# Optimization experiments

Hardware: AMD Instinct MI355X
Metric: run time of the kernel (lower is better)

The kernel has to match this reference:

```python
import jax, jax.numpy as jnp
import numpy as np

V, D, L, H, SLOTS, FF = 32000, 1024, 6, 16, 4096, 4096
DH = D // H

def rmsnorm(x, w, eps=1e-8):
    return x * jax.lax.rsqrt(jnp.mean(x * x, axis=-1, keepdims=True) + eps) * w

def rope(x):
    # x: [B,T,D]; interleaved RoPE over full d_model as in RoPEEmbedding
    T = x.shape[1]
    inv_freq = 1.0 / (10000.0 ** (jnp.arange(0, D, 2, dtype=jnp.float32) / D))
    freqs = jnp.arange(T, dtype=jnp.float32)[:, None] * inv_freq[None, :]  # [T, D/2]
    cos, sin = jnp.cos(freqs), jnp.sin(freqs)
    x1, x2 = x[..., ::2], x[..., 1::2]
    out = jnp.stack([x1 * cos - x2 * sin, x1 * sin + x2 * cos], axis=-1)
    return out.reshape(x.shape)

def block(x, Wq, Wk, Wv, Wo, bo, n1, Wg, Wu, Wd, n2):
    B, T, _ = x.shape
    q = (x @ Wq).reshape(B, T, H, DH)
    k = (x @ Wk).reshape(B, T, H, DH)
    v = (x @ Wv).reshape(B, T, H, DH)
    scores = jnp.einsum('bqhd,bkhd->bhqk', q, k) * (DH ** -0.5)
    attn = jax.nn.softmax(scores, axis=-1)
    o = jnp.einsum('bhqk,bkhd->bqhd', attn, v).reshape(B, T, D)
    x = rmsnorm(x + o @ Wo + bo, n1)
    ff = (jax.nn.silu(x @ Wg) * (x @ Wu)) @ Wd
    return rmsnorm(x + ff, n2)

def setup_inputs() -> dict:
    key = jax.random.key(0)
    ks = jax.random.split(key, 20)
    nrm = lambda k, s: (jax.random.normal(k, s, jnp.float32) * 0.02)
    inp = {
        'ids': jax.random.randint(ks[0], (2, 2048), 0, V),
        'tok_embed': nrm(ks[1], (V, D)),
        'Wq': nrm(ks[2], (L, D, D)), 'Wk': nrm(ks[3], (L, D, D)),
        'Wv': nrm(ks[4], (L, D, D)), 'Wo': nrm(ks[5], (L, D, D)),
        'bo': jnp.zeros((L, D), jnp.float32),
        'n1': jnp.ones((L, D), jnp.float32),
        'Wg': nrm(ks[6], (L, D, FF)), 'Wu': nrm(ks[7], (L, D, FF)),
        'Wd': nrm(ks[8], (L, FF, D)),
        'n2': jnp.ones((L, D), jnp.float32),
        'mem': nrm(ks[9], (SLOTS, D)),
        'Wsp': nrm(ks[10], (D, D)), 'bsp': jnp.zeros((D,), jnp.float32),
        'Wrp': nrm(ks[11], (D, D)), 'brp': jnp.zeros((D,), jnp.float32),
        'nout': jnp.ones((D,), jnp.float32),
    }
    return inp

def reference(ids, tok_embed, Wq, Wk, Wv, Wo, bo, n1, Wg, Wu, Wd, n2,
              mem, Wsp, bsp, Wrp, brp, nout):
    x = tok_embed[ids]            # [B,T,D] gather
    x = rope(x)
    for i in range(L):
        x = block(x, Wq[i], Wk[i], Wv[i], Wo[i], bo[i], n1[i],
                  Wg[i], Wu[i], Wd[i], n2[i])
    # StateBank content-addressed read: route queries over memory slots
    q = x @ Wsp + bsp                                   # [B,T,D]
    slot_scores = jnp.einsum('btd,sd->bts', q, mem) * (D ** -0.5)
    attention_maps = jax.nn.softmax(slot_scores, axis=-1)  # [B,T,SLOTS]
    r = jnp.einsum('bts,sd->btd', attention_maps, mem)     # gather-route read
    r = r @ Wrp + brp
    h = rmsnorm(x + r, nout)
    logits = h @ tok_embed.T      # tied lm_head
    return logits
```

## Files before the change

kernel.cpp:

```cpp
#include <hip/hip_runtime.h>

typedef __bf16 bf16;
typedef __attribute__((ext_vector_type(8))) __bf16 bf16x8;
typedef __attribute__((ext_vector_type(4))) __bf16 bf16x4;
typedef __attribute__((ext_vector_type(4))) float f32x4;

#define NL 6
#define DIM 1024
#define NH 16
#define DH 64
#define TT 2048
#define BB 2
#define BT 4096
#define FFD 4096
#define NSLOT 4096
#define NV 32000

__device__ __forceinline__ void gld16(const void* g, void* l) {
  __builtin_amdgcn_global_load_lds(
      (const __attribute__((address_space(1))) void*)g,
      (__attribute__((address_space(3))) void*)l, 16, 0, 0);
}


__global__ void cvt_bf16(const float* __restrict__ s, bf16* __restrict__ d, long n) {
  long i = ((long)blockIdx.x * 256 + threadIdx.x) * 4;
  if (i + 3 < n) {
    float4 v = *(const float4*)(s + i);
    bf16x4 o = {(bf16)v.x, (bf16)v.y, (bf16)v.z, (bf16)v.w};
    *(bf16x4*)(d + i) = o;
  }
}

__global__ void transpose_cvt(const float* __restrict__ src, bf16* __restrict__ dst, int R, int C) {
  __shared__ float tile[32][33];
  int c0 = blockIdx.x * 32, r0 = blockIdx.y * 32;
  int tx = threadIdx.x, ty = threadIdx.y;
#pragma unroll
  for (int i = 0; i < 4; ++i)
    tile[ty + i * 8][tx] = src[(size_t)(r0 + ty + i * 8) * C + c0 + tx];
  __syncthreads();
#pragma unroll
  for (int i = 0; i < 4; ++i)
    dst[(size_t)(c0 + ty + i * 8) * R + r0 + tx] = (bf16)tile[tx][ty + i * 8];
}

__global__ void transpose_v(const bf16* __restrict__ v, int ldv, bf16* __restrict__ vT) {
  __shared__ bf16 tile[32][33];
  int t0 = blockIdx.x * 32, d0 = blockIdx.y * 32, bh = blockIdx.z;
  int b = bh >> 4, h = bh & 15;
  int tx = threadIdx.x, ty = threadIdx.y;
#pragma unroll
  for (int i = 0; i < 4; ++i)
    tile[ty + i * 8][tx] = v[(size_t)(b * TT + t0 + ty + i * 8) * ldv + h * DH + d0 + tx];
  __syncthreads();
#pragma unroll
  for (int i = 0; i < 4; ++i)
    vT[((size_t)bh * DH + d0 + ty + i * 8) * TT + t0 + tx] = tile[tx][ty + i * 8];
}


__global__ void embed_rope(const int* __restrict__ ids, const float* __restrict__ emb,
                           float* __restrict__ xf, bf16* __restrict__ xb) {
  int bt = blockIdx.x;
  int t = bt & (TT - 1);
  int id = ids[bt];
  const float* row = emb + (size_t)id * DIM;
  for (int p = threadIdx.x; p < DIM / 2; p += 256) {
    float x1 = row[2 * p], x2 = row[2 * p + 1];
    float inv = __expf(-9.210340371976184f * (float)p * (1.0f / 512.0f));
    float ang = (float)t * inv;
    float c = cosf(ang), s = sinf(ang);
    float o1 = x1 * c - x2 * s;
    float o2 = x1 * s + x2 * c;
    size_t base = (size_t)bt * DIM + 2 * p;
    xf[base] = o1; xf[base + 1] = o2;
    xb[base] = (bf16)o1; xb[base + 1] = (bf16)o2;
  }
}


enum { EP_BF16 = 0, EP_F32 = 1, EP_F32_BIAS = 2, EP_BF16_BIAS = 3, EP_SILU_MUL = 4 };

template <int BM, int BN, int WMW, int WNW, int EP>
__global__ __launch_bounds__(WMW * WNW * 64, 2) void gemmk(
    const bf16* __restrict__ A, const bf16* __restrict__ Bt, void* __restrict__ Cp,
    const float* __restrict__ bias, const bf16* __restrict__ aux,
    int M, int N, int K) {
  constexpr int BK = 32;
  constexpr int NWAVE = WMW * WNW;
  constexpr int NTHR = NWAVE * 64;
  constexpr int MF = BM / (WMW * 16);
  constexpr int NF = BN / (WNW * 16);
  constexpr int AE = BM * BK;
  constexpr int BE = BN * BK;
  constexpr int RHALF = NTHR / 4;
  __shared__ bf16 sA[4][AE];
  __shared__ bf16 sB[4][BE];

  const int tid = threadIdx.x;
  const int lane = tid & 63;
  const int r16 = lane & 15, hi = lane >> 4;
  const int wave = tid >> 6;
  const int wm = wave / WNW, wn = wave % WNW;

  const int nwg = gridDim.x;
  const int orig = blockIdx.x;
  const int qq = nwg >> 3, rr = nwg & 7;
  const int xcd = orig & 7, cidx = orig >> 3;
  const int wg = (xcd < rr ? xcd * (qq + 1) : rr * (qq + 1) + (xcd - rr) * qq) + cidx;
  const int gM = M / BM;
  const int m0 = (wg % gM) * BM;
  const int n0 = (wg / gM) * BN;

  const int srow = tid >> 2;
  const int ccol = tid & 3;
  const int skey = (srow >> 1) & 3;
  const int gcol = ((ccol ^ skey)) * 8;
  const bf16* aS = A + (size_t)(m0 + srow) * K + gcol;
  const bf16* bS = Bt + (size_t)(n0 + srow) * K + gcol;
  const int dst0 = srow * BK + ccol * 8;

  const int rkey = (r16 >> 1) & 3;
  const int rchunk = (hi ^ rkey) * 8;

  f32x4 acc[MF][NF] = {};
  const int NT = K / BK;

  gld16(aS, &sA[0][dst0]);
  gld16(aS + (size_t)RHALF * K, &sA[0][dst0 + RHALF * BK]);
  gld16(bS, &sB[0][dst0]);
  gld16(bS + (size_t)RHALF * K, &sB[0][dst0 + RHALF * BK]);
  gld16(aS + BK, &sA[1][dst0]);
  gld16(aS + BK + (size_t)RHALF * K, &sA[1][dst0 + RHALF * BK]);
  gld16(bS + BK, &sB[1][dst0]);
  gld16(bS + BK + (size_t)RHALF * K, &sB[1][dst0 + RHALF * BK]);

  for (int t = 0; t < NT; ++t) {
    const int cb = t & 3;
    const int pb = (t + 2) & 3;
    const bool pre = (t + 2) < NT;
    if (pre) {
      gld16(aS + (size_t)(t + 2) * BK, &sA[pb][dst0]);
      gld16(aS + (size_t)(t + 2) * BK + (size_t)RHALF * K, &sA[pb][dst0 + RHALF * BK]);
    }
    if (pre)             asm volatile("s_waitcnt vmcnt(6)" ::: "memory");
    else if (t + 1 < NT) asm volatile("s_waitcnt vmcnt(4)" ::: "memory");
    else                 asm volatile("s_waitcnt vmcnt(0)" ::: "memory");
    __builtin_amdgcn_s_barrier();
    __builtin_amdgcn_sched_barrier(0);

    bf16x8 bf_[NF];
#pragma unroll
    for (int j = 0; j < NF; ++j)
      bf_[j] = *(const bf16x8*)&sB[cb][(wn * (NF * 16) + j * 16 + r16) * BK + rchunk];
    if (pre) {
      gld16(bS + (size_t)(t + 2) * BK, &sB[pb][dst0]);
      gld16(bS + (size_t)(t + 2) * BK + (size_t)RHALF * K, &sB[pb][dst0 + RHALF * BK]);
    }
    bf16x8 af[MF];
#pragma unroll
    for (int i = 0; i < MF; ++i)
      af[i] = *(const bf16x8*)&sA[cb][(wm * (MF * 16) + i * 16 + r16) * BK + rchunk];
    __builtin_amdgcn_s_setprio(1);
#pragma unroll
    for (int i = 0; i < MF; ++i)
#pragma unroll
      for (int j = 0; j < NF; ++j)
        acc[i][j] = __builtin_amdgcn_mfma_f32_16x16x32_bf16(af[i], bf_[j], acc[i][j], 0, 0, 0);
    __builtin_amdgcn_s_setprio(0);
  }

#pragma unroll
  for (int i = 0; i < MF; ++i) {
    const int m = m0 + wm * (MF * 16) + i * 16 + hi * 4;
#pragma unroll
    for (int j = 0; j < NF; ++j) {
      const int n = n0 + wn * (NF * 16) + j * 16 + r16;
#pragma unroll
      for (int q = 0; q < 4; ++q) {
        size_t idx = (size_t)(m + q) * N + n;
        float v = acc[i][j][q];
        if constexpr (EP == EP_F32) {
          ((float*)Cp)[idx] = v;
        } else if constexpr (EP == EP_F32_BIAS) {
          ((float*)Cp)[idx] = v + bias[n];
        } else if constexpr (EP == EP_BF16) {
          ((bf16*)Cp)[idx] = (bf16)v;
        } else if constexpr (EP == EP_BF16_BIAS) {
          ((bf16*)Cp)[idx] = (bf16)(v + bias[n]);
        } else {
          float sg = v / (1.0f + __expf(-v));
          ((bf16*)Cp)[idx] = (bf16)(sg * (float)aux[idx]);
        }
      }
    }
  }
}


__global__ __launch_bounds__(256, 2) void attn_flash(
    const bf16* __restrict__ Qp, const bf16* __restrict__ Kp, int ldk,
    const bf16* __restrict__ Vt, bf16* __restrict__ Op) {
  __shared__ bf16 Ks[2][128 * 32];
  __shared__ bf16 Vs[4][64 * 32];
  __shared__ bf16 Ps[4][4][16 * 40];
  const int tid = threadIdx.x, lane = tid & 63, wave = tid >> 6;
  const int h = blockIdx.y, b = blockIdx.z;
  const int r16 = lane & 15, hi = lane >> 4;
  const int qrow = blockIdx.x * 64 + wave * 16 + r16;

  bf16x8 qa[2];
  {
    const bf16* qp = Qp + (size_t)(b * TT + qrow) * ldk + h * DH + hi * 8;
    qa[0] = *(const bf16x8*)qp;
    qa[1] = *(const bf16x8*)(qp + 32);
  }
  const bf16* kBase = Kp + (size_t)(b * TT) * ldk + h * DH;
  const bf16* vBase = Vt + (size_t)(b * NH + h) * DH * TT;

  const int srow = tid >> 2, ccol = tid & 3;
  const int skey = (srow >> 1) & 3;
  const int scolS = (ccol ^ skey) * 8;
  const int dstc = ccol * 8;
  const int rkey = (r16 >> 1) & 3;
  const int rchunk = (hi ^ rkey) * 8;

  float m_run[4] = {-1e30f, -1e30f, -1e30f, -1e30f};
  float l_run[4] = {0.f, 0.f, 0.f, 0.f};
  f32x4 oacc[4] = {};

  for (int kt = 0; kt < TT; kt += 128) {
#pragma unroll
    for (int half = 0; half < 2; ++half) {
      gld16(kBase + (size_t)(kt + srow) * ldk + half * 32 + scolS, &Ks[half][srow * 32 + dstc]);
      gld16(kBase + (size_t)(kt + 64 + srow) * ldk + half * 32 + scolS, &Ks[half][(64 + srow) * 32 + dstc]);
    }
#pragma unroll
    for (int ks = 0; ks < 4; ++ks)
      gld16(vBase + (size_t)srow * TT + kt + ks * 32 + scolS, &Vs[ks][srow * 32 + dstc]);
    __syncthreads();

    f32x4 s[8];
#pragma unroll
    for (int kg = 0; kg < 8; ++kg) {
      f32x4 z = {};
      bf16x8 kb0 = *(const bf16x8*)&Ks[0][(kg * 16 + r16) * 32 + rchunk];
      bf16x8 kb1 = *(const bf16x8*)&Ks[1][(kg * 16 + r16) * 32 + rchunk];
      z = __builtin_amdgcn_mfma_f32_16x16x32_bf16(qa[0], kb0, z, 0, 0, 0);
      z = __builtin_amdgcn_mfma_f32_16x16x32_bf16(qa[1], kb1, z, 0, 0, 0);
      s[kg] = z * 0.125f;
    }
#pragma unroll
    for (int i = 0; i < 4; ++i) {
      float pm = s[0][i];
#pragma unroll
      for (int kg = 1; kg < 8; ++kg) pm = fmaxf(pm, s[kg][i]);
      pm = fmaxf(pm, __shfl_xor(pm, 1));
      pm = fmaxf(pm, __shfl_xor(pm, 2));
      pm = fmaxf(pm, __shfl_xor(pm, 4));
      pm = fmaxf(pm, __shfl_xor(pm, 8));
      float mnew = fmaxf(m_run[i], pm);
      float sc = __expf(m_run[i] - mnew);
      m_run[i] = mnew;
      l_run[i] *= sc;
#pragma unroll
      for (int n = 0; n < 4; ++n) oacc[n][i] *= sc;
#pragma unroll
      for (int kg = 0; kg < 8; ++kg) {
        float p = __expf(s[kg][i] - mnew);
        l_run[i] += p;
        Ps[wave][kg >> 1][(hi * 4 + i) * 40 + (kg & 1) * 16 + r16] = (bf16)p;
      }
    }
#pragma unroll
    for (int ks = 0; ks < 4; ++ks) {
      bf16x8 pa = *(const bf16x8*)&Ps[wave][ks][r16 * 40 + hi * 8];
#pragma unroll
      for (int n = 0; n < 4; ++n) {
        bf16x8 vb = *(const bf16x8*)&Vs[ks][(n * 16 + r16) * 32 + rchunk];
        oacc[n] = __builtin_amdgcn_mfma_f32_16x16x32_bf16(pa, vb, oacc[n], 0, 0, 0);
      }
    }
    __syncthreads();
  }

#pragma unroll
  for (int i = 0; i < 4; ++i) {
    float l = l_run[i];
    l += __shfl_xor(l, 1);
    l += __shfl_xor(l, 2);
    l += __shfl_xor(l, 4);
    l += __shfl_xor(l, 8);
    float inv = 1.0f / l;
    int trow = blockIdx.x * 64 + wave * 16 + hi * 4 + i;
    size_t base = ((size_t)b * TT + trow) * DIM + h * DH;
#pragma unroll
    for (int n = 0; n < 4; ++n)
      Op[base + n * 16 + r16] = (bf16)(oacc[n][i] * inv);
  }
}


__global__ __launch_bounds__(256) void resid_rms(
    const float* __restrict__ xin, const float* __restrict__ y, const float* __restrict__ wgt,
    float* __restrict__ xf_out, bf16* __restrict__ xb_out) {
  __shared__ float red[4];
  const int r = blockIdx.x, tid = threadIdx.x;
  const size_t base = (size_t)r * DIM + tid * 4;
  float4 v = *(const float4*)(xin + base);
  float4 u = *(const float4*)(y + base);
  v.x += u.x; v.y += u.y; v.z += u.z; v.w += u.w;
  float ss = v.x * v.x + v.y * v.y + v.z * v.z + v.w * v.w;
#pragma unroll
  for (int d = 1; d < 64; d <<= 1) ss += __shfl_xor(ss, d);
  if ((tid & 63) == 0) red[tid >> 6] = ss;
  __syncthreads();
  ss = red[0] + red[1] + red[2] + red[3];
  float sc = rsqrtf(ss * (1.0f / DIM) + 1e-8f);
  const float4 wv = *(const float4*)(wgt + tid * 4);
  float o0 = v.x * sc * wv.x, o1 = v.y * sc * wv.y, o2 = v.z * sc * wv.z, o3 = v.w * sc * wv.w;
  if (xf_out) {
    float4 ov = {o0, o1, o2, o3};
    *(float4*)(xf_out + base) = ov;
  }
  bf16x4 ob = {(bf16)o0, (bf16)o1, (bf16)o2, (bf16)o3};
  *(bf16x4*)(xb_out + base) = ob;
}


__global__ __launch_bounds__(256) void softmax_rows(const float* __restrict__ Sc, bf16* __restrict__ P) {
  __shared__ float red[4];
  const int r = blockIdx.x, tid = threadIdx.x;
  const float* row = Sc + (size_t)r * NSLOT;
  float4 v[4];
#pragma unroll
  for (int i = 0; i < 4; ++i) v[i] = *(const float4*)(row + tid * 4 + i * 1024);
  float mx = -1e30f;
#pragma unroll
  for (int i = 0; i < 4; ++i)
    mx = fmaxf(fmaxf(fmaxf(fmaxf(mx, v[i].x), v[i].y), v[i].z), v[i].w);
#pragma unroll
  for (int d = 1; d < 64; d <<= 1) mx = fmaxf(mx, __shfl_xor(mx, d));
  if ((tid & 63) == 0) red[tid >> 6] = mx;
  __syncthreads();
  mx = fmaxf(fmaxf(red[0], red[1]), fmaxf(red[2], red[3]));
  __syncthreads();
  float e[16];
  float sum = 0.f;
#pragma unroll
  for (int i = 0; i < 4; ++i) {
    e[i * 4 + 0] = __expf((v[i].x - mx) * 0.03125f);
    e[i * 4 + 1] = __expf((v[i].y - mx) * 0.03125f);
    e[i * 4 + 2] = __expf((v[i].z - mx) * 0.03125f);
    e[i * 4 + 3] = __expf((v[i].w - mx) * 0.03125f);
    sum += e[i * 4 + 0] + e[i * 4 + 1] + e[i * 4 + 2] + e[i * 4 + 3];
  }
#pragma unroll
  for (int d = 1; d < 64; d <<= 1) sum += __shfl_xor(sum, d);
  if ((tid & 63) == 0) red[tid >> 6] = sum;
  __syncthreads();
  sum = red[0] + red[1] + red[2] + red[3];
  float inv = 1.0f / sum;
#pragma unroll
  for (int i = 0; i < 4; ++i) {
    bf16x4 ob = {(bf16)(e[i * 4 + 0] * inv), (bf16)(e[i * 4 + 1] * inv),
                 (bf16)(e[i * 4 + 2] * inv), (bf16)(e[i * 4 + 3] * inv)};
    *(bf16x4*)(P + (size_t)r * NSLOT + tid * 4 + i * 1024) = ob;
  }
}


extern "C" void kernel_launch(void* const* d_in, const int* in_sizes, int n_in,
                              void* d_out, int out_size, void* d_ws, size_t ws_size,
                              hipStream_t stream) {
  (void)in_sizes; (void)n_in; (void)out_size;
  const int* ids = (const int*)d_in[0];
  const float* emb = (const float*)d_in[1];
  const float* Wq = (const float*)d_in[2];
  const float* Wk = (const float*)d_in[3];
  const float* Wv = (const float*)d_in[4];
  const float* Wo = (const float*)d_in[5];
  const float* bo = (const float*)d_in[6];
  const float* n1 = (const float*)d_in[7];
  const float* Wg = (const float*)d_in[8];
  const float* Wu = (const float*)d_in[9];
  const float* Wd = (const float*)d_in[10];
  const float* n2 = (const float*)d_in[11];
  const float* memp = (const float*)d_in[12];
  const float* Wsp = (const float*)d_in[13];
  const float* bsp = (const float*)d_in[14];
  const float* Wrp = (const float*)d_in[15];
  const float* brp = (const float*)d_in[16];
  const float* nout = (const float*)d_in[17];

  char* w = (char*)d_ws;
  auto alloc = [&](size_t bytes) -> void* {
    void* p = (void*)w;
    w += (bytes + 255) & ~(size_t)255;
    return p;
  };

  const size_t dd = (size_t)DIM * DIM;
  const size_t dff = (size_t)DIM * FFD;

  bf16* tok_b = (bf16*)alloc((size_t)NV * DIM * 2);
  bf16* mem_b = (bf16*)alloc((size_t)NSLOT * DIM * 2);
  bf16* memT  = (bf16*)alloc((size_t)NSLOT * DIM * 2);
  bf16* WspT  = (bf16*)alloc(dd * 2);
  bf16* WrpT  = (bf16*)alloc(dd * 2);
  float* xf   = (float*)alloc((size_t)BT * DIM * 4);
  bf16* xb    = (bf16*)alloc((size_t)BT * DIM * 2);
  float* yb   = (float*)alloc((size_t)BT * DIM * 4);
  bf16* W3T   = (bf16*)alloc(3 * dd * 2);
  bf16* WoT   = (bf16*)alloc(dd * 2);
  bf16* WgT   = (bf16*)alloc(dff * 2);
  bf16* WuT   = (bf16*)alloc(dff * 2);
  bf16* WdT   = (bf16*)alloc(dff * 2);
  bf16* qkv   = (bf16*)alloc((size_t)BT * 3 * DIM * 2);
  bf16* vT_   = (bf16*)alloc((size_t)BT * DIM * 2);
  bf16* ot_   = (bf16*)alloc((size_t)BT * DIM * 2);
  bf16* qb    = (bf16*)alloc((size_t)BT * DIM * 2);
  bf16* rb    = (bf16*)alloc((size_t)BT * DIM * 2);
  bf16* hb    = (bf16*)alloc((size_t)BT * DIM * 2);

  size_t used = (size_t)(w - (char*)d_ws);
  size_t region_bytes = (size_t)BT * NSLOT * 4 + (size_t)BT * NSLOT * 2;
  char* region;
  if (used + region_bytes <= ws_size) region = (char*)alloc(region_bytes);
  else region = (char*)d_out;
  bf16* Ub = (bf16*)region;
  bf16* Hb = (bf16*)(region + (size_t)BT * FFD * 2);
  float* scoresF = (float*)region;
  bf16* attnb = (bf16*)(region + (size_t)BT * NSLOT * 4);

  dim3 blkT(32, 8);

  cvt_bf16<<<NV * DIM / 1024, 256, 0, stream>>>(emb, tok_b, (long)NV * DIM);
  cvt_bf16<<<NSLOT * DIM / 1024, 256, 0, stream>>>(memp, mem_b, (long)NSLOT * DIM);
  transpose_cvt<<<dim3(DIM / 32, NSLOT / 32), blkT, 0, stream>>>(memp, memT, NSLOT, DIM);
  transpose_cvt<<<dim3(DIM / 32, DIM / 32), blkT, 0, stream>>>(Wsp, WspT, DIM, DIM);
  transpose_cvt<<<dim3(DIM / 32, DIM / 32), blkT, 0, stream>>>(Wrp, WrpT, DIM, DIM);
  embed_rope<<<BT, 256, 0, stream>>>(ids, emb, xf, xb);

  for (int l = 0; l < NL; ++l) {
    transpose_cvt<<<dim3(32, 32), blkT, 0, stream>>>(Wq + l * dd, W3T, DIM, DIM);
    transpose_cvt<<<dim3(32, 32), blkT, 0, stream>>>(Wk + l * dd, W3T + dd, DIM, DIM);
    transpose_cvt<<<dim3(32, 32), blkT, 0, stream>>>(Wv + l * dd, W3T + 2 * dd, DIM, DIM);
    transpose_cvt<<<dim3(32, 32), blkT, 0, stream>>>(Wo + l * dd, WoT, DIM, DIM);
    transpose_cvt<<<dim3(FFD / 32, DIM / 32), blkT, 0, stream>>>(Wg + l * dff, WgT, DIM, FFD);
    transpose_cvt<<<dim3(FFD / 32, DIM / 32), blkT, 0, stream>>>(Wu + l * dff, WuT, DIM, FFD);
    transpose_cvt<<<dim3(DIM / 32, FFD / 32), blkT, 0, stream>>>(Wd + l * dff, WdT, FFD, DIM);

    gemmk<128, 128, 2, 2, EP_BF16><<<dim3(32 * 24), 256, 0, stream>>>(
        xb, W3T, qkv, nullptr, nullptr, BT, 3 * DIM, DIM);
    transpose_v<<<dim3(TT / 32, DH / 32, BB * NH), blkT, 0, stream>>>(qkv + 2 * DIM, 3 * DIM, vT_);
    attn_flash<<<dim3(TT / 64, NH, BB), 256, 0, stream>>>(qkv, qkv + DIM, 3 * DIM, vT_, ot_);
    gemmk<128, 128, 2, 2, EP_F32_BIAS><<<dim3(8 * 32), 256, 0, stream>>>(
        ot_, WoT, yb, bo + l * DIM, nullptr, BT, DIM, DIM);
    resid_rms<<<BT, 256, 0, stream>>>(xf, yb, n1 + l * DIM, xf, xb);
    gemmk<256, 256, 2, 4, EP_BF16><<<dim3(16 * 16), 512, 0, stream>>>(
        xb, WuT, Ub, nullptr, nullptr, BT, FFD, DIM);
    gemmk<256, 256, 2, 4, EP_SILU_MUL><<<dim3(16 * 16), 512, 0, stream>>>(
        xb, WgT, Hb, nullptr, Ub, BT, FFD, DIM);
    gemmk<128, 128, 2, 2, EP_F32><<<dim3(8 * 32), 256, 0, stream>>>(
        Hb, WdT, yb, nullptr, nullptr, BT, DIM, FFD);
    resid_rms<<<BT, 256, 0, stream>>>(xf, yb, n2 + l * DIM, xf, xb);
  }

  gemmk<128, 128, 2, 2, EP_BF16_BIAS><<<dim3(8 * 32), 256, 0, stream>>>(
      xb, WspT, qb, bsp, nullptr, BT, DIM, DIM);
  gemmk<256, 256, 2, 4, EP_F32><<<dim3(16 * 16), 512, 0, stream>>>(
      qb, mem_b, scoresF, nullptr, nullptr, BT, NSLOT, DIM);
  softmax_rows<<<BT, 256, 0, stream>>>(scoresF, attnb);
  gemmk<128, 128, 2, 2, EP_BF16><<<dim3(8 * 32), 256, 0, stream>>>(
      attnb, memT, rb, nullptr, nullptr, BT, DIM, NSLOT);
  gemmk<128, 128, 2, 2, EP_F32_BIAS><<<dim3(8 * 32), 256, 0, stream>>>(
      rb, WrpT, yb, brp, nullptr, BT, DIM, DIM);
  resid_rms<<<BT, 256, 0, stream>>>(xf, yb, nout, nullptr, hb);
  gemmk<256, 256, 2, 4, EP_F32><<<dim3(16 * 125), 512, 0, stream>>>(
      hb, tok_b, (float*)d_out, nullptr, nullptr, BT, NV, DIM);
}
```

Measured before the change: 3.072 ms.

## Add 8-wave 256x256 GEMM kernel with ping-pong phased MFMA/load scheduling

Adds a new gemm8 kernel with 256x256 tiles, BK=64, and 8 waves. Its main loop is split into four phases that interleave global-to-LDS async loads with MFMA bursts, using barriers, s_setprio and explicit vmcnt waits. It also applies an XOR swizzle to the LDS layout and remaps workgroups by XCD. It replaces the large GEMMs (QKV, FFN up/gate, slot scores, lm_head), aiming to keep matrix units busy while loads are in flight. The cost is one workgroup per CU, and the code relies on N being divisible by 256, which may not hold for lm_head N=32000.

```diff
diff --git a/kernel.cpp b/kernel.cpp
--- a/kernel.cpp
+++ b/kernel.cpp
@@ -79,8 +79,140 @@
   }
 }
 
-
 enum { EP_BF16 = 0, EP_F32 = 1, EP_F32_BIAS = 2, EP_BF16_BIAS = 3, EP_SILU_MUL = 4 };
+
+
+#define GPHASE(KS, MH, LOADB, STG, WAITC)                                         \
+  {                                                                               \
+    if (LOADB) {                                                                  \
+      _Pragma("unroll") for (int j = 0; j < 4; ++j)                               \
+          bfr[j] = *(const bf16x8*)&SB[(KS)*8192 + (wn*64 + j*16 + r16)*32 + rchunk]; \
+    }                                                                             \
+    _Pragma("unroll") for (int i = 0; i < 4; ++i)                                 \
+        af[i] = *(const bf16x8*)&SA[(KS)*8192 + (wm*128 + (MH)*64 + i*16 + r16)*32 + rchunk]; \
+    STG;                                                                          \
+    __builtin_amdgcn_s_barrier();                                                 \
+    __builtin_amdgcn_sched_barrier(0);                                            \
+    __builtin_amdgcn_s_setprio(1);                                                \
+    _Pragma("unroll") for (int i = 0; i < 4; ++i)                                 \
+        _Pragma("unroll") for (int j = 0; j < 4; ++j)                             \
+            acc[(MH)*4 + i][j] = __builtin_amdgcn_mfma_f32_16x16x32_bf16(         \
+                af[i], bfr[j], acc[(MH)*4 + i][j], 0, 0, 0);                      \
+    __builtin_amdgcn_s_setprio(0);                                                \
+    WAITC;                                                                        \
+    __builtin_amdgcn_s_barrier();                                                 \
+    __builtin_amdgcn_sched_barrier(0);                                            \
+  }
+
+template <int EP>
+__global__ __launch_bounds__(512, 1) void gemm8(
+    const bf16* __restrict__ A, const bf16* __restrict__ Bt, void* __restrict__ Cp,
+    const float* __restrict__ bias, const bf16* __restrict__ aux,
+    int M, int N, int K) {
+  constexpr int BK = 64;
+  __shared__ bf16 Ssh[2 * 2 * 2 * 256 * 32];
+
+  const int tid = threadIdx.x;
+  const int lane = tid & 63;
+  const int r16 = lane & 15, hi = lane >> 4;
+  const int wave = tid >> 6;
+  const int wm = wave >> 2, wn = wave & 3;
+
+  const int nwg = gridDim.x;
+  const int orig = blockIdx.x;
+  const int qq = nwg >> 3, rr = nwg & 7;
+  const int xcd = orig & 7, cidx = orig >> 3;
+  const int wg = (xcd < rr ? xcd * (qq + 1) : rr * (qq + 1) + (xcd - rr) * qq) + cidx;
+  const int gM = M / 256;
+  const int m0 = (wg % gM) * 256;
+  const int n0 = (wg / gM) * 256;
+
+  const int srow = tid >> 2;
+  const int ccol = tid & 3;
+  const int skey = (srow >> 1) & 3;
+  const int gcol = (ccol ^ skey) * 8;
+  const bf16* aS = A + (size_t)(m0 + srow) * K + gcol;
+  const bf16* bS = Bt + (size_t)(n0 + srow) * K + gcol;
+  const int dst0 = srow * 32 + ccol * 8;
+
+  const int rkey = (r16 >> 1) & 3;
+  const int rchunk = (hi ^ rkey) * 8;
+
+  f32x4 acc[8][4] = {};
+  const int NT = K / BK;
+
+  {
+    bf16* S0A = Ssh;
+    bf16* S0B = Ssh + 16384;
+    gld16(aS, S0A + dst0);
+    gld16(aS + (size_t)128 * K, S0A + 4096 + dst0);
+    gld16(bS, S0B + dst0);
+    gld16(bS + (size_t)128 * K, S0B + 4096 + dst0);
+    gld16(aS + 32, S0A + 8192 + dst0);
+    gld16(aS + 32 + (size_t)128 * K, S0A + 8192 + 4096 + dst0);
+    gld16(bS + 32, S0B + 8192 + dst0);
+    gld16(bS + 32 + (size_t)128 * K, S0B + 8192 + 4096 + dst0);
+    asm volatile("s_waitcnt vmcnt(4)" ::: "memory");
+    __builtin_amdgcn_s_barrier();
+    __builtin_amdgcn_sched_barrier(0);
+  }
+
+  for (int t = 0; t < NT; ++t) {
+    const int cb = t & 1, nb = cb ^ 1;
+    const bool pre = (t + 1) < NT;
+    const size_t koff = (size_t)(t + 1) * BK;
+    bf16* SA = Ssh + cb * 32768;
+    bf16* SB = SA + 16384;
+    bf16* NA = Ssh + nb * 32768;
+    bf16* NB = NA + 16384;
+    bf16x8 af[4], bfr[4];
+
+    GPHASE(0, 0, true,
+      { if (pre) { gld16(aS + koff, NA + dst0);
+                   gld16(aS + koff + (size_t)128 * K, NA + 4096 + dst0); } },
+      {});
+    GPHASE(0, 1, false,
+      { if (pre) { gld16(bS + koff, NB + dst0);
+                   gld16(bS + koff + (size_t)128 * K, NB + 4096 + dst0); } },
+      { if (pre) asm volatile("s_waitcnt vmcnt(4)" ::: "memory");
+        else     asm volatile("s_waitcnt vmcnt(0)" ::: "memory"); });
+    GPHASE(1, 0, true,
+      { if (pre) { gld16(aS + koff + 32, NA + 8192 + dst0);
+                   gld16(aS + koff + 32 + (size_t)128 * K, NA + 8192 + 4096 + dst0); } },
+      {});
+    GPHASE(1, 1, false,
+      { if (pre) { gld16(bS + koff + 32, NB + 8192 + dst0);
+                   gld16(bS + koff + 32 + (size_t)128 * K, NB + 8192 + 4096 + dst0); } },
+      { if (pre) asm volatile("s_waitcnt vmcnt(4)" ::: "memory"); });
+  }
+
+#pragma unroll
+  for (int mi = 0; mi < 8; ++mi) {
+    const int m = m0 + wm * 128 + mi * 16 + hi * 4;
+#pragma unroll
+    for (int j = 0; j < 4; ++j) {
+      const int n = n0 + wn * 64 + j * 16 + r16;
+#pragma unroll
+      for (int q = 0; q < 4; ++q) {
+        size_t idx = (size_t)(m + q) * N + n;
+        float v = acc[mi][j][q];
+        if constexpr (EP == EP_F32) {
+          ((float*)Cp)[idx] = v;
+        } else if constexpr (EP == EP_F32_BIAS) {
+          ((float*)Cp)[idx] = v + bias[n];
+        } else if constexpr (EP == EP_BF16) {
+          ((bf16*)Cp)[idx] = (bf16)v;
+        } else if constexpr (EP == EP_BF16_BIAS) {
+          ((bf16*)Cp)[idx] = (bf16)(v + bias[n]);
+        } else {
+          float sg = v / (1.0f + __expf(-v));
+          ((bf16*)Cp)[idx] = (bf16)(sg * (float)aux[idx]);
+        }
+      }
+    }
+  }
+}
+
 
 template <int BM, int BN, int WMW, int WNW, int EP>
 __global__ __launch_bounds__(WMW * WNW * 64, 2) void gemmk(
@@ -452,16 +584,16 @@
     transpose_cvt<<<dim3(FFD / 32, DIM / 32), blkT, 0, stream>>>(Wu + l * dff, WuT, DIM, FFD);
     transpose_cvt<<<dim3(DIM / 32, FFD / 32), blkT, 0, stream>>>(Wd + l * dff, WdT, FFD, DIM);
 
-    gemmk<128, 128, 2, 2, EP_BF16><<<dim3(32 * 24), 256, 0, stream>>>(
+    gemm8<EP_BF16><<<dim3(16 * 12), 512, 0, stream>>>(
         xb, W3T, qkv, nullptr, nullptr, BT, 3 * DIM, DIM);
     transpose_v<<<dim3(TT / 32, DH / 32, BB * NH), blkT, 0, stream>>>(qkv + 2 * DIM, 3 * DIM, vT_);
     attn_flash<<<dim3(TT / 64, NH, BB), 256, 0, stream>>>(qkv, qkv + DIM, 3 * DIM, vT_, ot_);
     gemmk<128, 128, 2, 2, EP_F32_BIAS><<<dim3(8 * 32), 256, 0, stream>>>(
         ot_, WoT, yb, bo + l * DIM, nullptr, BT, DIM, DIM);
     resid_rms<<<BT, 256, 0, stream>>>(xf, yb, n1 + l * DIM, xf, xb);
-    gemmk<256, 256, 2, 4, EP_BF16><<<dim3(16 * 16), 512, 0, stream>>>(
+    gemm8<EP_BF16><<<dim3(16 * 16), 512, 0, stream>>>(
         xb, WuT, Ub, nullptr, nullptr, BT, FFD, DIM);
-    gemmk<256, 256, 2, 4, EP_SILU_MUL><<<dim3(16 * 16), 512, 0, stream>>>(
+    gemm8<EP_SILU_MUL><<<dim3(16 * 16), 512, 0, stream>>>(
         xb, WgT, Hb, nullptr, Ub, BT, FFD, DIM);
     gemmk<128, 128, 2, 2, EP_F32><<<dim3(8 * 32), 256, 0, stream>>>(
         Hb, WdT, yb, nullptr, nullptr, BT, DIM, FFD);
@@ -470,7 +602,7 @@
 
   gemmk<128, 128, 2, 2, EP_BF16_BIAS><<<dim3(8 * 32), 256, 0, stream>>>(
       xb, WspT, qb, bsp, nullptr, BT, DIM, DIM);
-  gemmk<256, 256, 2, 4, EP_F32><<<dim3(16 * 16), 512, 0, stream>>>(
+  gemm8<EP_F32><<<dim3(16 * 16), 512, 0, stream>>>(
       qb, mem_b, scoresF, nullptr, nullptr, BT, NSLOT, DIM);
   softmax_rows<<<BT, 256, 0, stream>>>(scoresF, attnb);
   gemmk<128, 128, 2, 2, EP_BF16><<<dim3(8 * 32), 256, 0, stream>>>(
@@ -478,6 +610,6 @@
   gemmk<128, 128, 2, 2, EP_F32_BIAS><<<dim3(8 * 32), 256, 0, stream>>>(
       rb, WrpT, yb, brp, nullptr, BT, DIM, DIM);
   resid_rms<<<BT, 256, 0, stream>>>(xf, yb, nout, nullptr, hb);
-  gemmk<256, 256, 2, 4, EP_F32><<<dim3(16 * 125), 512, 0, stream>>>(
+  gemm8<EP_F32><<<dim3(16 * 125), 512, 0, stream>>>(
       hb, tok_b, (float*)d_out, nullptr, nullptr, BT, NV, DIM);
 }
```

After: 2.918 ms. 5.0% less time.
